# Kernel tuning notes

Measured on AMD Instinct MI355X. Metric: run time of the kernel, lower is better.

## Reference

```python
import jax, jax.numpy as jnp
import numpy as np

C_MID = 32  # inChannels // 8
# Packing order matches torch loop: diagonal offset -i for i in 0..C-1,
# i.e. pairs (j+i, j) for j in 0..C-1-i, concatenated.
_ROWS = np.concatenate([np.arange(C_MID - i) + i for i in range(C_MID)])
_COLS = np.concatenate([np.arange(C_MID - i) for i in range(C_MID)])


def _bn_relu(y, g, b, m, v, eps=1e-5):
    # y: (B, C, H, W); per-channel affine BN (eval-style) + relu
    inv = g / jnp.sqrt(v + eps)
    return jax.nn.relu(y * inv[:, None, None] + (b - m * inv)[:, None, None])


def setup_inputs() -> dict:
    key = jax.random.key(0)
    ks = jax.random.split(key, 14)
    B, Cin, H, W = 16, 256, 64, 64
    mid, T, Cout = C_MID, C_MID * (C_MID + 1) // 2, 256
    return {
        "x": jax.random.normal(ks[0], (B, Cin, H, W), jnp.float32),
        "w1": jax.random.normal(ks[1], (mid, Cin), jnp.float32) * 0.05,
        "b1": jax.random.normal(ks[2], (mid,), jnp.float32) * 0.05,
        "g1": jax.random.uniform(ks[3], (mid,), jnp.float32, 0.5, 1.5),
        "be1": jax.random.normal(ks[4], (mid,), jnp.float32) * 0.1,
        "m1": jax.random.normal(ks[5], (mid,), jnp.float32) * 0.1,
        "v1": jax.random.uniform(ks[6], (mid,), jnp.float32, 0.5, 1.5),
        "w2": jax.random.normal(ks[7], (Cout, T), jnp.float32) * 0.05,
        "b2": jax.random.normal(ks[8], (Cout,), jnp.float32) * 0.05,
        "g2": jax.random.uniform(ks[9], (Cout,), jnp.float32, 0.5, 1.5),
        "be2": jax.random.normal(ks[10], (Cout,), jnp.float32) * 0.1,
        "m2": jax.random.normal(ks[11], (Cout,), jnp.float32) * 0.1,
        "v2": jax.random.uniform(ks[12], (Cout,), jnp.float32, 0.5, 1.5),
    }


def reference(x, w1, b1, g1, be1, m1, v1, w2, b2, g2, be2, m2, v2):
    # dimReduceLayer1: 1x1 conv + BN + relu
    y = jnp.einsum('bchw,oc->bohw', x, w1) + b1[:, None, None]
    y = _bn_relu(y, g1, be1, m1, v1)                       # (B, mid, H, W)
    yb = jnp.transpose(y, (0, 2, 3, 1))                    # (B, H, W, mid)
    rows = jnp.asarray(_ROWS)
    cols = jnp.asarray(_COLS)
    # Packed lower-triangular bilinear features, exactly the torch diagonal+cat order.
    packed = yb[..., rows] * yb[..., cols]                 # (B, H, W, T)
    # dimReduceLayer2: 1x1 conv + BN + relu
    z = jnp.einsum('bhwt,ot->bohw', packed, w2) + b2[:, None, None]
    return _bn_relu(z, g2, be2, m2, v2)
```

## Files before the change

kernel.cpp:

```cpp
#include <hip/hip_runtime.h>

#define EPS 1e-5f

typedef float f32x4 __attribute__((ext_vector_type(4)));
typedef short bf16x8 __attribute__((ext_vector_type(8)));

__device__ __forceinline__ unsigned short f2bf(float f) {
  unsigned int u = __builtin_bit_cast(unsigned int, f);
  u = (u + 0x7FFFu + ((u >> 16) & 1u)) >> 16;
  return (unsigned short)u;
}

__global__ __launch_bounds__(256) void k_prep(
    const float* __restrict__ w1, const float* __restrict__ b1,
    const float* __restrict__ g1, const float* __restrict__ be1,
    const float* __restrict__ m1, const float* __restrict__ v1,
    const float* __restrict__ w2, const float* __restrict__ b2,
    const float* __restrict__ g2, const float* __restrict__ be2,
    const float* __restrict__ m2, const float* __restrict__ v2,
    float* __restrict__ beta1, float* __restrict__ beta2,
    unsigned short* __restrict__ w1b, unsigned short* __restrict__ w2f)
{
  int t = blockIdx.x * 256 + threadIdx.x;
  if (t < 139264) {
    int j = t & 7, l = (t >> 3) & 63, g = t >> 9;
    int ct = g & 15, ks = g >> 4;
    int k = ks * 32 + (l >> 4) * 8 + j;
    int ch = ct * 16 + (l & 15);
    float val = 0.f;
    if (k < 528) {
      float s2 = g2[ch] * rsqrtf(v2[ch] + EPS);
      val = w2[ch * 528 + k] * s2;
    }
    w2f[t] = f2bf(val);
  }
  if (t < 8192) {
    int j = t & 7, l = (t >> 3) & 63, g = t >> 9;
    int ct = g & 1, ks = g >> 1;
    int c = ks * 32 + (l >> 4) * 8 + j;
    int m = ct * 16 + (l & 15);
    float s1 = g1[m] * rsqrtf(v1[m] + EPS);
    w1b[t] = f2bf(w1[m * 256 + c] * s1);
  }
  if (t < 32) {
    float s1 = g1[t] * rsqrtf(v1[t] + EPS);
    beta1[t] = (b1[t] - m1[t]) * s1 + be1[t];
  }
  if (t < 256) {
    float s2 = g2[t] * rsqrtf(v2[t] + EPS);
    beta2[t] = (b2[t] - m2[t]) * s2 + be2[t];
  }
}

template<int I>
__device__ __forceinline__ void do_diag(const float* __restrict__ y,
                                        unsigned short* __restrict__ pr)
{
  constexpr int L = 32 - I;
  constexpr int base = 32 * I - (I * (I - 1)) / 2;
  float p[L];
#pragma unroll
  for (int j = 0; j < L; ++j) p[j] = y[I + j] * y[j];
  constexpr int s = (base & 1) ? 1 : 0;
  if constexpr (s != 0) pr[base] = f2bf(p[0]);
#pragma unroll
  for (int j = s; j + 1 < L; j += 2)
    *(unsigned int*)&pr[base + j] =
        (unsigned int)f2bf(p[j]) | ((unsigned int)f2bf(p[j + 1]) << 16);
  if constexpr (((L - s) & 1) != 0) pr[base + L - 1] = f2bf(p[L - 1]);
}

template<int S>
__device__ __forceinline__ void do_set(const float* __restrict__ y,
                                       unsigned short* __restrict__ pr)
{
  do_diag<S>(y, pr);
  do_diag<31 - S>(y, pr);
  do_diag<S + 8>(y, pr);
  do_diag<23 - S>(y, pr);
}

__global__ __launch_bounds__(256, 4) void k_fused(
    const float* __restrict__ x, const unsigned short* __restrict__ w1b,
    const float* __restrict__ beta1, const unsigned short* __restrict__ w2f,
    const float* __restrict__ beta2, float* __restrict__ out)
{
  __shared__ __align__(16) unsigned short pk[32 * 548];
  __shared__ __align__(8) float yf[32 * 34];
  int tid = threadIdx.x;
  int wv = tid >> 6, lane = tid & 63;
  int l15 = lane & 15, l4 = lane >> 4;
  int pb = blockIdx.x * 32;
  int b = pb >> 12, hw0 = pb & 4095;
  const float* xb = x + ((size_t)b << 20) + hw0;

  unsigned short* xt = pk;
  {
    int q = tid & 7;
    int cg = tid >> 3;
#pragma unroll
    for (int pass = 0; pass < 2; ++pass) {
      int c4 = cg + pass * 32;
      float4 v[4];
#pragma unroll
      for (int i = 0; i < 4; ++i)
        v[i] = *(const float4*)&xb[(size_t)(4 * c4 + i) * 4096 + 4 * q];
#pragma unroll
      for (int s = 0; s < 4; ++s) {
        float e0 = ((const float*)&v[0])[s];
        float e1 = ((const float*)&v[1])[s];
        float e2 = ((const float*)&v[2])[s];
        float e3 = ((const float*)&v[3])[s];
        unsigned int lo = (unsigned int)f2bf(e0) | ((unsigned int)f2bf(e1) << 16);
        unsigned int hi = (unsigned int)f2bf(e2) | ((unsigned int)f2bf(e3) << 16);
        *(uint2*)&xt[(4 * q + s) * 276 + 4 * c4] = make_uint2(lo, hi);
      }
    }
  }
  __syncthreads();

  {
    int pxt = wv & 1, mt = wv >> 1;
    int px = pxt * 16 + l15;
    f32x4 acc1 = (f32x4){0.f, 0.f, 0.f, 0.f};
    const uint4* w1b4 = (const uint4*)w1b;
    for (int ks = 0; ks < 8; ++ks) {
      union { uint4 q; bf16x8 v; } A, B;
      A.q = w1b4[(ks * 2 + mt) * 64 + lane];
      const unsigned short* s = &xt[px * 276 + ks * 32 + l4 * 8];
      uint2 lo = *(const uint2*)s;
      uint2 hi = *(const uint2*)(s + 4);
      B.q = make_uint4(lo.x, lo.y, hi.x, hi.y);
      acc1 = __builtin_amdgcn_mfma_f32_16x16x32_bf16(A.v, B.v, acc1, 0, 0, 0);
    }
    int m0 = mt * 16 + l4 * 4;
#pragma unroll
    for (int r = 0; r < 4; ++r)
      yf[px * 34 + m0 + r] = fmaxf(acc1[r] + beta1[m0 + r], 0.f);
  }
  __syncthreads();

  {
    int px2 = tid & 31, set = tid >> 5;
    const float* yr = &yf[px2 * 34];
    unsigned short* pr = &pk[px2 * 548];
    float y[32];
#pragma unroll
    for (int k = 0; k < 16; ++k) {
      float2 v = *(const float2*)&yr[2 * k];
      y[2 * k] = v.x; y[2 * k + 1] = v.y;
    }
    switch (set) {
      case 0: do_set<0>(y, pr); break;
      case 1: do_set<1>(y, pr); break;
      case 2: do_set<2>(y, pr); break;
      case 3: do_set<3>(y, pr); break;
      case 4: do_set<4>(y, pr); break;
      case 5: do_set<5>(y, pr); break;
      case 6: do_set<6>(y, pr); break;
      default: do_set<7>(y, pr); break;
    }
    if (set < 4) {
      *(unsigned int*)&pr[528 + set * 4] = 0u;
      *(unsigned int*)&pr[530 + set * 4] = 0u;
    }
  }
  __syncthreads();

  f32x4 acc[2][4];
#pragma unroll
  for (int a = 0; a < 2; ++a)
#pragma unroll
    for (int c = 0; c < 4; ++c)
      acc[a][c] = (f32x4){0.f, 0.f, 0.f, 0.f};

  const uint4* w2f4 = (const uint4*)w2f;
  for (int ks = 0; ks < 17; ++ks) {
    union { uint4 q; bf16x8 v; } A[4], B[2];
#pragma unroll
    for (int ctl = 0; ctl < 4; ++ctl)
      A[ctl].q = w2f4[(ks * 16 + wv * 4 + ctl) * 64 + lane];
#pragma unroll
    for (int pt = 0; pt < 2; ++pt) {
      const unsigned short* src = &pk[(pt * 16 + l15) * 548 + ks * 32 + l4 * 8];
      uint2 lo = *(const uint2*)src;
      uint2 hi = *(const uint2*)(src + 4);
      B[pt].q = make_uint4(lo.x, lo.y, hi.x, hi.y);
    }
#pragma unroll
    for (int pt = 0; pt < 2; ++pt)
#pragma unroll
      for (int ctl = 0; ctl < 4; ++ctl)
        acc[pt][ctl] = __builtin_amdgcn_mfma_f32_16x16x32_bf16(
            A[ctl].v, B[pt].v, acc[pt][ctl], 0, 0, 0);
  }

  float bet[4][4];
#pragma unroll
  for (int ctl = 0; ctl < 4; ++ctl)
#pragma unroll
    for (int r = 0; r < 4; ++r)
      bet[ctl][r] = beta2[(wv * 4 + ctl) * 16 + l4 * 4 + r];

#pragma unroll
  for (int pt = 0; pt < 2; ++pt) {
    int hw = hw0 + pt * 16 + l15;
#pragma unroll
    for (int ctl = 0; ctl < 4; ++ctl) {
      int ch = (wv * 4 + ctl) * 16 + l4 * 4;
#pragma unroll
      for (int r = 0; r < 4; ++r) {
        float v = fmaxf(acc[pt][ctl][r] + bet[ctl][r], 0.f);
        out[(((size_t)b * 256 + (ch + r)) << 12) + hw] = v;
      }
    }
  }
}

extern "C" void kernel_launch(void* const* d_in, const int* in_sizes, int n_in,
                              void* d_out, int out_size, void* d_ws, size_t ws_size,
                              hipStream_t stream)
{
  const float* x   = (const float*)d_in[0];
  const float* w1  = (const float*)d_in[1];
  const float* b1  = (const float*)d_in[2];
  const float* g1  = (const float*)d_in[3];
  const float* be1 = (const float*)d_in[4];
  const float* m1  = (const float*)d_in[5];
  const float* v1  = (const float*)d_in[6];
  const float* w2  = (const float*)d_in[7];
  const float* b2  = (const float*)d_in[8];
  const float* g2  = (const float*)d_in[9];
  const float* be2 = (const float*)d_in[10];
  const float* m2  = (const float*)d_in[11];
  const float* v2  = (const float*)d_in[12];

  char* ws = (char*)d_ws;
  float*          beta1 = (float*)(ws);
  float*          beta2 = (float*)(ws + 128);
  unsigned short* w1b   = (unsigned short*)(ws + 1152);
  unsigned short* w2f   = (unsigned short*)(ws + 17536);
  float* out = (float*)d_out;

  k_prep<<<dim3(544), dim3(256), 0, stream>>>(
      w1, b1, g1, be1, m1, v1, w2, b2, g2, be2, m2, v2, beta1, beta2, w1b, w2f);
  k_fused<<<dim3(2048), dim3(256), 0, stream>>>(x, w1b, beta1, w2f, beta2, out);
}
```

Measured before the change: 48.62 us.

## Double threads per block and split fused kernel work across eight waves

The fused kernel moves from 256 to 512 threads per block, and each stage's work is split across twice as many waves. The x transpose needs one pass instead of two. Each thread now builds two diagonals of the bilinear products instead of four, and each wave computes two output channel tiles instead of four in the second GEMM. The intent is more waves in flight to hide memory and LDS latency, plus fewer registers per thread. In exchange, the first GEMM is computed redundantly by waves 4-7 (they write the same values), and the tighter launch bounds may force register spilling.

```diff
diff --git a/kernel.cpp b/kernel.cpp
--- a/kernel.cpp
+++ b/kernel.cpp
@@ -71,16 +71,14 @@
 }
 
 template<int S>
-__device__ __forceinline__ void do_set(const float* __restrict__ y,
-                                       unsigned short* __restrict__ pr)
+__device__ __forceinline__ void do_pair(const float* __restrict__ y,
+                                        unsigned short* __restrict__ pr)
 {
   do_diag<S>(y, pr);
   do_diag<31 - S>(y, pr);
-  do_diag<S + 8>(y, pr);
-  do_diag<23 - S>(y, pr);
-}
-
-__global__ __launch_bounds__(256, 4) void k_fused(
+}
+
+__global__ __launch_bounds__(512, 8) void k_fused(
     const float* __restrict__ x, const unsigned short* __restrict__ w1b,
     const float* __restrict__ beta1, const unsigned short* __restrict__ w2f,
     const float* __restrict__ beta2, float* __restrict__ out)
@@ -97,33 +95,31 @@
   unsigned short* xt = pk;
   {
     int q = tid & 7;
-    int cg = tid >> 3;
-#pragma unroll
-    for (int pass = 0; pass < 2; ++pass) {
-      int c4 = cg + pass * 32;
-      float4 v[4];
-#pragma unroll
-      for (int i = 0; i < 4; ++i)
-        v[i] = *(const float4*)&xb[(size_t)(4 * c4 + i) * 4096 + 4 * q];
-#pragma unroll
-      for (int s = 0; s < 4; ++s) {
-        float e0 = ((const float*)&v[0])[s];
-        float e1 = ((const float*)&v[1])[s];
-        float e2 = ((const float*)&v[2])[s];
-        float e3 = ((const float*)&v[3])[s];
-        unsigned int lo = (unsigned int)f2bf(e0) | ((unsigned int)f2bf(e1) << 16);
-        unsigned int hi = (unsigned int)f2bf(e2) | ((unsigned int)f2bf(e3) << 16);
-        *(uint2*)&xt[(4 * q + s) * 276 + 4 * c4] = make_uint2(lo, hi);
-      }
+    int c4 = tid >> 3;
+    float4 v[4];
+#pragma unroll
+    for (int i = 0; i < 4; ++i)
+      v[i] = *(const float4*)&xb[(size_t)(4 * c4 + i) * 4096 + 4 * q];
+#pragma unroll
+    for (int s = 0; s < 4; ++s) {
+      float e0 = ((const float*)&v[0])[s];
+      float e1 = ((const float*)&v[1])[s];
+      float e2 = ((const float*)&v[2])[s];
+      float e3 = ((const float*)&v[3])[s];
+      unsigned int lo = (unsigned int)f2bf(e0) | ((unsigned int)f2bf(e1) << 16);
+      unsigned int hi = (unsigned int)f2bf(e2) | ((unsigned int)f2bf(e3) << 16);
+      *(uint2*)&xt[(4 * q + s) * 276 + 4 * c4] = make_uint2(lo, hi);
     }
   }
   __syncthreads();
 
   {
-    int pxt = wv & 1, mt = wv >> 1;
+    int t = wv & 3;
+    int pxt = t & 1, mt = t >> 1;
     int px = pxt * 16 + l15;
     f32x4 acc1 = (f32x4){0.f, 0.f, 0.f, 0.f};
     const uint4* w1b4 = (const uint4*)w1b;
+#pragma unroll
     for (int ks = 0; ks < 8; ++ks) {
       union { uint4 q; bf16x8 v; } A, B;
       A.q = w1b4[(ks * 2 + mt) * 64 + lane];
@@ -151,35 +147,53 @@
       y[2 * k] = v.x; y[2 * k + 1] = v.y;
     }
     switch (set) {
-      case 0: do_set<0>(y, pr); break;
-      case 1: do_set<1>(y, pr); break;
-      case 2: do_set<2>(y, pr); break;
-      case 3: do_set<3>(y, pr); break;
-      case 4: do_set<4>(y, pr); break;
-      case 5: do_set<5>(y, pr); break;
-      case 6: do_set<6>(y, pr); break;
-      default: do_set<7>(y, pr); break;
+      case 0:  do_pair<0>(y, pr);  break;
+      case 1:  do_pair<1>(y, pr);  break;
+      case 2:  do_pair<2>(y, pr);  break;
+      case 3:  do_pair<3>(y, pr);  break;
+      case 4:  do_pair<4>(y, pr);  break;
+      case 5:  do_pair<5>(y, pr);  break;
+      case 6:  do_pair<6>(y, pr);  break;
+      case 7:  do_pair<7>(y, pr);  break;
+      case 8:  do_pair<8>(y, pr);  break;
+      case 9:  do_pair<9>(y, pr);  break;
+      case 10: do_pair<10>(y, pr); break;
+      case 11: do_pair<11>(y, pr); break;
+      case 12: do_pair<12>(y, pr); break;
+      case 13: do_pair<13>(y, pr); break;
+      case 14: do_pair<14>(y, pr); break;
+      default: do_pair<15>(y, pr); break;
     }
     if (set < 4) {
       *(unsigned int*)&pr[528 + set * 4] = 0u;
       *(unsigned int*)&pr[530 + set * 4] = 0u;
     }
   }
+
+  float bet[2][4];
+#pragma unroll
+  for (int ci = 0; ci < 2; ++ci)
+#pragma unroll
+    for (int r = 0; r < 4; ++r)
+      bet[ci][r] = beta2[(wv * 2 + ci) * 16 + l4 * 4 + r];
+
   __syncthreads();
 
-  f32x4 acc[2][4];
+  f32x4 acc[2][2];
 #pragma unroll
   for (int a = 0; a < 2; ++a)
 #pragma unroll
-    for (int c = 0; c < 4; ++c)
+    for (int c = 0; c < 2; ++c)
       acc[a][c] = (f32x4){0.f, 0.f, 0.f, 0.f};
 
   const uint4* w2f4 = (const uint4*)w2f;
+  int wbase = wv * 2;
+#pragma unroll
   for (int ks = 0; ks < 17; ++ks) {
-    union { uint4 q; bf16x8 v; } A[4], B[2];
-#pragma unroll
-    for (int ctl = 0; ctl < 4; ++ctl)
-      A[ctl].q = w2f4[(ks * 16 + wv * 4 + ctl) * 64 + lane];
+    union { uint4 q; bf16x8 v; } A[2], B[2];
+#pragma unroll
+    for (int ci = 0; ci < 2; ++ci)
+      A[ci].q = w2f4[(ks * 16 + wbase + ci) * 64 + lane];
 #pragma unroll
     for (int pt = 0; pt < 2; ++pt) {
       const unsigned short* src = &pk[(pt * 16 + l15) * 548 + ks * 32 + l4 * 8];
@@ -190,27 +204,20 @@
 #pragma unroll
     for (int pt = 0; pt < 2; ++pt)
 #pragma unroll
-      for (int ctl = 0; ctl < 4; ++ctl)
-        acc[pt][ctl] = __builtin_amdgcn_mfma_f32_16x16x32_bf16(
-            A[ctl].v, B[pt].v, acc[pt][ctl], 0, 0, 0);
-  }
-
-  float bet[4][4];
-#pragma unroll
-  for (int ctl = 0; ctl < 4; ++ctl)
-#pragma unroll
-    for (int r = 0; r < 4; ++r)
-      bet[ctl][r] = beta2[(wv * 4 + ctl) * 16 + l4 * 4 + r];
+      for (int ci = 0; ci < 2; ++ci)
+        acc[pt][ci] = __builtin_amdgcn_mfma_f32_16x16x32_bf16(
+            A[ci].v, B[pt].v, acc[pt][ci], 0, 0, 0);
+  }
 
 #pragma unroll
   for (int pt = 0; pt < 2; ++pt) {
     int hw = hw0 + pt * 16 + l15;
 #pragma unroll
-    for (int ctl = 0; ctl < 4; ++ctl) {
-      int ch = (wv * 4 + ctl) * 16 + l4 * 4;
+    for (int ci = 0; ci < 2; ++ci) {
+      int ch = (wbase + ci) * 16 + l4 * 4;
 #pragma unroll
       for (int r = 0; r < 4; ++r) {
-        float v = fmaxf(acc[pt][ctl][r] + bet[ctl][r], 0.f);
+        float v = fmaxf(acc[pt][ci][r] + bet[ci][r], 0.f);
         out[(((size_t)b * 256 + (ch + r)) << 12) + hw] = v;
       }
     }
@@ -244,5 +251,5 @@
 
   k_prep<<<dim3(544), dim3(256), 0, stream>>>(
       w1, b1, g1, be1, m1, v1, w2, b2, g2, be2, m2, v2, beta1, beta2, w1b, w2f);
-  k_fused<<<dim3(2048), dim3(256), 0, stream>>>(x, w1b, beta1, w2f, beta2, out);
-}
+  k_fused<<<dim3(2048), dim3(512), 0, stream>>>(x, w1b, beta1, w2f, beta2, out);
+}
```

Result: slower. 52.29 us (+7.5%).
